# Kernel optimization log

Hardware: AMD Instinct MI355X
Metric: run time of the kernel (lower is better)

Reference implementation:

```python
import jax, jax.numpy as jnp
import numpy as np

B, E, F, N = 4, 800_000, 128, 100_000  # batch, elements, features, num segments
NEG_SLOPE = 0.2


def setup_inputs() -> dict:
    key = jax.random.key(0)
    k1, k2, k3 = jax.random.split(key, 3)
    x = jax.random.normal(k1, (B, E, F), dtype=jnp.float32)
    W = jax.random.normal(k2, (F, 1), dtype=jnp.float32) * (1.0 / np.sqrt(F))
    b = jnp.zeros((1,), dtype=jnp.float32)
    idx = jax.random.randint(k3, (E,), 0, N, dtype=jnp.int32)
    return {"x": x, "W": W, "b": b, "idx": idx}


def reference(x, W, b, idx):
    # linear: [B,E,F] @ [F,1] + [1] -> [B,E,1]
    s = jnp.einsum('bef,fo->beo', x, W) + b
    # LeakyReLU(negative_slope=0.2)
    s = jnp.where(s >= 0, s, NEG_SLOPE * s)
    # scatter_softmax over dim=1 grouped by idx (numerically stable)
    s2 = s[..., 0].T                                   # [E, B]
    m = jax.ops.segment_max(s2, idx, num_segments=N)   # [N, B] per-segment max
    e = jnp.exp(s2 - m[idx])                           # [E, B]
    den = jax.ops.segment_sum(e, idx, num_segments=N)  # [N, B]
    out = e / den[idx]                                 # [E, B]
    return out.T[..., None]                            # [B, E, 1]
```

## Files before the change

kernel.cpp:

```cpp
#include <hip/hip_runtime.h>
#include <math.h>

#define BB 4
#define EE 800000
#define FF 128
#define NSEG 100000
#define NEG_SLOPE 0.2f
#define TOTAL (BB * EE)
#define NGRP (TOTAL / 8)

typedef float f4 __attribute__((ext_vector_type(4)));

__global__ void init_den(float* __restrict__ den) {
    int i = blockIdx.x * blockDim.x + threadIdx.x;
    if (i < NSEG * BB) den[i] = 0.0f;
}

__global__ void __launch_bounds__(256)
linear_exp_sum(const float* __restrict__ x,
               const float* __restrict__ W,
               const float* __restrict__ bias,
               const int* __restrict__ idx,
               float* __restrict__ out,
               float* __restrict__ den) {
    const int lane = threadIdx.x & 63;
    const int waveId = (blockIdx.x * blockDim.x + threadIdx.x) >> 6;
    const int nWaves = (gridDim.x * blockDim.x) >> 6;

    const f4 wf = reinterpret_cast<const f4*>(W)[lane & 31];
    const float bv = bias[0];
    const f4* x4 = reinterpret_cast<const f4*>(x);

    for (int g = waveId; g < NGRP; g += nWaves) {
        const f4* p = x4 + (long long)g * 256 + lane;
        const f4 v0 = __builtin_nontemporal_load(p);
        const f4 v1 = __builtin_nontemporal_load(p + 64);
        const f4 v2 = __builtin_nontemporal_load(p + 128);
        const f4 v3 = __builtin_nontemporal_load(p + 192);

        float p0 = v0.x * wf.x + v0.y * wf.y + v0.z * wf.z + v0.w * wf.w;
        float p1 = v1.x * wf.x + v1.y * wf.y + v1.z * wf.z + v1.w * wf.w;
        float p2 = v2.x * wf.x + v2.y * wf.y + v2.z * wf.z + v2.w * wf.w;
        float p3 = v3.x * wf.x + v3.y * wf.y + v3.z * wf.z + v3.w * wf.w;

        const float a01 = p0 + __shfl_xor(p0, 1);
        const float b01 = p1 + __shfl_xor(p1, 1);
        const float a23 = p2 + __shfl_xor(p2, 1);
        const float b23 = p3 + __shfl_xor(p3, 1);
        float t01 = (lane & 1) ? b01 : a01;
        float t23 = (lane & 1) ? b23 : a23;
        const float u01 = t01 + __shfl_xor(t01, 2);
        const float u23 = t23 + __shfl_xor(t23, 2);
        float u = (lane & 2) ? u23 : u01;
        u += __shfl_xor(u, 4);
        u += __shfl_xor(u, 8);
        u += __shfl_xor(u, 16);

        if ((lane & 31) < 4) {
            const int off = ((lane & 3) << 1) | (lane >> 5);
            const int base = g * 8;
            const int b = base / EE;
            const int r = base - b * EE + off;
            float a = u + bv;
            a = (a >= 0.0f) ? a : NEG_SLOPE * a;
            const float ev = __expf(a);
            out[base + off] = ev;
            atomicAdd(&den[idx[r] * BB + b], ev);
        }
    }
}

__global__ void norm_kernel(const int* __restrict__ idx,
                            const float* __restrict__ den,
                            float* __restrict__ out) {
    const int e = blockIdx.x * blockDim.x + threadIdx.x;
    if (e >= EE) return;
    const int n = idx[e];
    const f4 d = reinterpret_cast<const f4*>(den)[n];
    out[0 * EE + e] /= d.x;
    out[1 * EE + e] /= d.y;
    out[2 * EE + e] /= d.z;
    out[3 * EE + e] /= d.w;
}

extern "C" void kernel_launch(void* const* d_in, const int* in_sizes, int n_in,
                              void* d_out, int out_size, void* d_ws, size_t ws_size,
                              hipStream_t stream) {
    const float* x    = (const float*)d_in[0];
    const float* W    = (const float*)d_in[1];
    const float* bias = (const float*)d_in[2];
    const int*   idx  = (const int*)d_in[3];
    float* out = (float*)d_out;

    float* den = (float*)d_ws;

    {
        const int total = NSEG * BB;
        init_den<<<(total + 255) / 256, 256, 0, stream>>>(den);
    }
    {
        linear_exp_sum<<<2048, 256, 0, stream>>>(x, W, bias, idx, out, den);
    }
    {
        norm_kernel<<<(EE + 255) / 256, 256, 0, stream>>>(idx, den, out);
    }
}
```

Before: 319.2 us.

## Fuse init, linear-exp-sum and normalize into one cooperative kernel with grid syncs

Replaces three separate kernel launches with one cooperative kernel that zeroes the denominators, computes the linear+LeakyReLU+exp with atomic segment sums, and normalizes, separated by two grid-wide syncs. The aim is to remove launch overhead and inter-kernel gaps. In exchange, the grid is capped at 1024 blocks for co-residency, which halves the grid used by the main streaming phase, and each grid sync adds barrier cost.

Result: slower. 494.5 us (+54.9%).

```diff
diff --git a/kernel.cpp b/kernel.cpp
--- a/kernel.cpp
+++ b/kernel.cpp
@@ -1,5 +1,8 @@
 #include <hip/hip_runtime.h>
+#include <hip/hip_cooperative_groups.h>
 #include <math.h>
+
+namespace cg = cooperative_groups;
 
 #define BB 4
 #define EE 800000
@@ -9,78 +12,84 @@
 #define TOTAL (BB * EE)
 #define NGRP (TOTAL / 8)
 
+#define NBLK 1024
+#define NTHR 256
+
 typedef float f4 __attribute__((ext_vector_type(4)));
 
-__global__ void init_den(float* __restrict__ den) {
-    int i = blockIdx.x * blockDim.x + threadIdx.x;
-    if (i < NSEG * BB) den[i] = 0.0f;
-}
+__global__ void __launch_bounds__(NTHR)
+fused_attn(const float* __restrict__ x,
+           const float* __restrict__ W,
+           const float* __restrict__ bias,
+           const int* __restrict__ idx,
+           float* __restrict__ out,
+           float* __restrict__ den) {
+    cg::grid_group grid = cg::this_grid();
+    const int tid = blockIdx.x * blockDim.x + threadIdx.x;
+    const int nThreads = NBLK * NTHR;
 
-__global__ void __launch_bounds__(256)
-linear_exp_sum(const float* __restrict__ x,
-               const float* __restrict__ W,
-               const float* __restrict__ bias,
-               const int* __restrict__ idx,
-               float* __restrict__ out,
-               float* __restrict__ den) {
-    const int lane = threadIdx.x & 63;
-    const int waveId = (blockIdx.x * blockDim.x + threadIdx.x) >> 6;
-    const int nWaves = (gridDim.x * blockDim.x) >> 6;
+    for (int i = tid; i < NSEG * BB; i += nThreads) den[i] = 0.0f;
 
-    const f4 wf = reinterpret_cast<const f4*>(W)[lane & 31];
-    const float bv = bias[0];
-    const f4* x4 = reinterpret_cast<const f4*>(x);
+    grid.sync();
 
-    for (int g = waveId; g < NGRP; g += nWaves) {
-        const f4* p = x4 + (long long)g * 256 + lane;
-        const f4 v0 = __builtin_nontemporal_load(p);
-        const f4 v1 = __builtin_nontemporal_load(p + 64);
-        const f4 v2 = __builtin_nontemporal_load(p + 128);
-        const f4 v3 = __builtin_nontemporal_load(p + 192);
+    {
+        const int lane = threadIdx.x & 63;
+        const int waveId = tid >> 6;
+        const int nWaves = nThreads >> 6;
 
-        float p0 = v0.x * wf.x + v0.y * wf.y + v0.z * wf.z + v0.w * wf.w;
-        float p1 = v1.x * wf.x + v1.y * wf.y + v1.z * wf.z + v1.w * wf.w;
-        float p2 = v2.x * wf.x + v2.y * wf.y + v2.z * wf.z + v2.w * wf.w;
-        float p3 = v3.x * wf.x + v3.y * wf.y + v3.z * wf.z + v3.w * wf.w;
+        const f4 wf = reinterpret_cast<const f4*>(W)[lane & 31];
+        const float bv = bias[0];
+        const f4* x4 = reinterpret_cast<const f4*>(x);
 
-        const float a01 = p0 + __shfl_xor(p0, 1);
-        const float b01 = p1 + __shfl_xor(p1, 1);
-        const float a23 = p2 + __shfl_xor(p2, 1);
-        const float b23 = p3 + __shfl_xor(p3, 1);
-        float t01 = (lane & 1) ? b01 : a01;
-        float t23 = (lane & 1) ? b23 : a23;
-        const float u01 = t01 + __shfl_xor(t01, 2);
-        const float u23 = t23 + __shfl_xor(t23, 2);
-        float u = (lane & 2) ? u23 : u01;
-        u += __shfl_xor(u, 4);
-        u += __shfl_xor(u, 8);
-        u += __shfl_xor(u, 16);
+        for (int g = waveId; g < NGRP; g += nWaves) {
+            const f4* p = x4 + (long long)g * 256 + lane;
+            const f4 v0 = __builtin_nontemporal_load(p);
+            const f4 v1 = __builtin_nontemporal_load(p + 64);
+            const f4 v2 = __builtin_nontemporal_load(p + 128);
+            const f4 v3 = __builtin_nontemporal_load(p + 192);
 
-        if ((lane & 31) < 4) {
-            const int off = ((lane & 3) << 1) | (lane >> 5);
-            const int base = g * 8;
-            const int b = base / EE;
-            const int r = base - b * EE + off;
-            float a = u + bv;
-            a = (a >= 0.0f) ? a : NEG_SLOPE * a;
-            const float ev = __expf(a);
-            out[base + off] = ev;
-            atomicAdd(&den[idx[r] * BB + b], ev);
+            float p0 = v0.x * wf.x + v0.y * wf.y + v0.z * wf.z + v0.w * wf.w;
+            float p1 = v1.x * wf.x + v1.y * wf.y + v1.z * wf.z + v1.w * wf.w;
+            float p2 = v2.x * wf.x + v2.y * wf.y + v2.z * wf.z + v2.w * wf.w;
+            float p3 = v3.x * wf.x + v3.y * wf.y + v3.z * wf.z + v3.w * wf.w;
+
+            const float a01 = p0 + __shfl_xor(p0, 1);
+            const float b01 = p1 + __shfl_xor(p1, 1);
+            const float a23 = p2 + __shfl_xor(p2, 1);
+            const float b23 = p3 + __shfl_xor(p3, 1);
+            float t01 = (lane & 1) ? b01 : a01;
+            float t23 = (lane & 1) ? b23 : a23;
+            const float u01 = t01 + __shfl_xor(t01, 2);
+            const float u23 = t23 + __shfl_xor(t23, 2);
+            float u = (lane & 2) ? u23 : u01;
+            u += __shfl_xor(u, 4);
+            u += __shfl_xor(u, 8);
+            u += __shfl_xor(u, 16);
+
+            if ((lane & 31) < 4) {
+                const int off = ((lane & 3) << 1) | (lane >> 5);
+                const int base = g * 8;
+                const int b = base / EE;
+                const int r = base - b * EE + off;
+                float a = u + bv;
+                a = (a >= 0.0f) ? a : NEG_SLOPE * a;
+                const float ev = __expf(a);
+                out[base + off] = ev;
+                atomicAdd(&den[idx[r] * BB + b], ev);
+            }
         }
     }
-}
 
-__global__ void norm_kernel(const int* __restrict__ idx,
-                            const float* __restrict__ den,
-                            float* __restrict__ out) {
-    const int e = blockIdx.x * blockDim.x + threadIdx.x;
-    if (e >= EE) return;
-    const int n = idx[e];
-    const f4 d = reinterpret_cast<const f4*>(den)[n];
-    out[0 * EE + e] /= d.x;
-    out[1 * EE + e] /= d.y;
-    out[2 * EE + e] /= d.z;
-    out[3 * EE + e] /= d.w;
+    grid.sync();
+
+    for (int e = tid; e < EE; e += nThreads) {
+        const int n = idx[e];
+        const f4 d = reinterpret_cast<const f4*>(den)[n];
+        out[0 * EE + e] /= d.x;
+        out[1 * EE + e] /= d.y;
+        out[2 * EE + e] /= d.z;
+        out[3 * EE + e] /= d.w;
+    }
 }
 
 extern "C" void kernel_launch(void* const* d_in, const int* in_sizes, int n_in,
@@ -91,17 +100,10 @@
     const float* bias = (const float*)d_in[2];
     const int*   idx  = (const int*)d_in[3];
     float* out = (float*)d_out;
-
     float* den = (float*)d_ws;
 
-    {
-        const int total = NSEG * BB;
-        init_den<<<(total + 255) / 256, 256, 0, stream>>>(den);
-    }
-    {
-        linear_exp_sum<<<2048, 256, 0, stream>>>(x, W, bias, idx, out, den);
-    }
-    {
-        norm_kernel<<<(EE + 255) / 256, 256, 0, stream>>>(idx, den, out);
-    }
+    void* args[] = {(void*)&x, (void*)&W, (void*)&bias, (void*)&idx,
+                    (void*)&out, (void*)&den};
+    hipLaunchCooperativeKernel((void*)fused_attn, dim3(NBLK), dim3(NTHR),
+                               args, 0, stream);
 }
```
